# Performance work log

Measured on AMD Instinct MI355X. Metric: run time of the kernel, lower is better.

Reference implementation:

```python
import jax, jax.numpy as jnp
import numpy as np

C = 128
EPS = 1e-5


def _ln(x, g, b):
    m = jnp.mean(x, axis=-1, keepdims=True)
    v = jnp.mean((x - m) ** 2, axis=-1, keepdims=True)
    return (x - m) * jax.lax.rsqrt(v + EPS) * g + b


def setup_inputs() -> dict:
    key = jax.random.key(0)
    ks = jax.random.split(key, 10)
    B, N = 1, 384
    s = 1.0 / np.sqrt(C)
    inp = {
        "z": jax.random.normal(ks[0], (B, N, N, C), dtype=jnp.float32),
        "ln1_g": jnp.ones((C,), jnp.float32),
        "ln1_b": jnp.zeros((C,), jnp.float32),
        "ln2_g": jnp.ones((C,), jnp.float32),
        "ln2_b": jnp.zeros((C,), jnp.float32),
        "Wa": jax.random.uniform(ks[1], (C, C), jnp.float32, -s, s),
        "ba": jnp.zeros((C,), jnp.float32),
        "Wga": jax.random.uniform(ks[2], (C, C), jnp.float32, -s, s),
        "bga": jnp.zeros((C,), jnp.float32),
        "Wb": jax.random.uniform(ks[3], (C, C), jnp.float32, -s, s),
        "bb": jnp.zeros((C,), jnp.float32),
        "Wgb": jax.random.uniform(ks[4], (C, C), jnp.float32, -s, s),
        "bgb": jnp.zeros((C,), jnp.float32),
        "Wg": jax.random.uniform(ks[5], (C, C), jnp.float32, -s, s),
        "bg": jnp.zeros((C,), jnp.float32),
        "Wo": jax.random.uniform(ks[6], (C, C), jnp.float32, -s, s),
        "bo": jnp.zeros((C,), jnp.float32),
    }
    return inp


def reference(z, ln1_g, ln1_b, ln2_g, ln2_b, Wa, ba, Wga, bga, Wb, bb, Wgb, bgb, Wg, bg, Wo, bo):
    # z: (B, i, j, c)
    zn = _ln(z, ln1_g, ln1_b)
    a = (zn @ Wa + ba) * jax.nn.sigmoid(zn @ Wga + bga)      # (B,i,k,c)
    b = (zn @ Wb + bb) * jax.nn.sigmoid(zn @ Wgb + bgb)      # (B,j,k,c)
    gate = jax.nn.sigmoid(zn @ Wg + bg)                      # (B,i,j,c)
    o = jnp.einsum('bikc,bjkc->bijc', a, b)                  # outgoing triangle update
    return gate * (_ln(o, ln2_g, ln2_b) @ Wo + bo)
```

## Files before the change

kernel.cpp:

```cpp
#include <hip/hip_runtime.h>
#include <stdint.h>

typedef _Float16 f16x8 __attribute__((ext_vector_type(8)));
typedef float floatx4 __attribute__((ext_vector_type(4)));

#define RR 147456
#define NC 128
#define NN 384

__device__ inline floatx4 zero4() { floatx4 v; v[0]=0.f; v[1]=0.f; v[2]=0.f; v[3]=0.f; return v; }
__device__ inline float sigmoidf_(float x) { return 1.f / (1.f + __expf(-x)); }

__global__ __launch_bounds__(256) void k0_wt(
    const float* __restrict__ w0, const float* __restrict__ w1,
    const float* __restrict__ w2, const float* __restrict__ w3,
    const float* __restrict__ w4, const float* __restrict__ w5,
    _Float16* __restrict__ wf)
{
  const float* w;
  switch (blockIdx.x) {
    case 0: w = w0; break; case 1: w = w1; break; case 2: w = w2; break;
    case 3: w = w3; break; case 4: w = w4; break; default: w = w5; break;
  }
  _Float16* out = wf + blockIdx.x * 16384;
  const int t = threadIdx.x;
  for (int it = 0; it < 64; ++it) {
    int f = it * 256 + t;
    int j  = f & 7;
    int ln = (f >> 3) & 63;
    int nt = (f >> 9) & 7;
    int k0 = f >> 12;
    int k = k0 * 32 + (ln >> 4) * 8 + j;
    int n = nt * 16 + (ln & 15);
    out[f] = (_Float16)w[k * 128 + n];
  }
}

__global__ __launch_bounds__(256, 4) void k2_ln_gemm(
    const float* __restrict__ z, const float* __restrict__ ln1g, const float* __restrict__ ln1b,
    const _Float16* __restrict__ wf,
    const float* __restrict__ ba, const float* __restrict__ bga,
    const float* __restrict__ bb, const float* __restrict__ bgb,
    const float* __restrict__ bg,
    _Float16* __restrict__ at, _Float16* __restrict__ bt, _Float16* __restrict__ gate)
{
  __shared__ __align__(16) _Float16 zns[64][136];
  __shared__ __align__(16) _Float16 bnc[4][32 * 72];
  const int t = threadIdx.x;
  const int w = t >> 6, lane = t & 63;
  const int l15 = lane & 15, quad = lane >> 4;
  const int r0 = blockIdx.x * 64;
  const int nt0 = w * 2;

  {
    const int g = lane >> 4, h = lane & 15;
    float4 ga = *(const float4*)(ln1g + h*8);
    float4 gb = *(const float4*)(ln1g + h*8 + 4);
    float4 bba = *(const float4*)(ln1b + h*8);
    float4 bbb = *(const float4*)(ln1b + h*8 + 4);
    #pragma unroll
    for (int rr = 0; rr < 4; ++rr) {
      int row = w * 16 + rr * 4 + g;
      const float* zp = z + (size_t)(r0 + row) * NC + h * 8;
      float4 xa = *(const float4*)zp;
      float4 xb = *(const float4*)(zp + 4);
      float s = xa.x + xa.y + xa.z + xa.w + xb.x + xb.y + xb.z + xb.w;
      float q = xa.x*xa.x + xa.y*xa.y + xa.z*xa.z + xa.w*xa.w
              + xb.x*xb.x + xb.y*xb.y + xb.z*xb.z + xb.w*xb.w;
      #pragma unroll
      for (int m = 1; m < 16; m <<= 1) { s += __shfl_xor(s, m); q += __shfl_xor(q, m); }
      float mean = s * (1.f/128.f);
      float var  = q * (1.f/128.f) - mean*mean;
      float rs = rsqrtf(var + 1e-5f);
      union { uint4 u; _Float16 hh[8]; } pk;
      pk.hh[0] = (_Float16)((xa.x - mean) * rs * ga.x + bba.x);
      pk.hh[1] = (_Float16)((xa.y - mean) * rs * ga.y + bba.y);
      pk.hh[2] = (_Float16)((xa.z - mean) * rs * ga.z + bba.z);
      pk.hh[3] = (_Float16)((xa.w - mean) * rs * ga.w + bba.w);
      pk.hh[4] = (_Float16)((xb.x - mean) * rs * gb.x + bbb.x);
      pk.hh[5] = (_Float16)((xb.y - mean) * rs * gb.y + bbb.y);
      pk.hh[6] = (_Float16)((xb.z - mean) * rs * gb.z + bbb.z);
      pk.hh[7] = (_Float16)((xb.w - mean) * rs * gb.w + bbb.w);
      *(uint4*)&zns[row][h * 8] = pk.u;
    }
  }
  __syncthreads();

  const _Float16* pw = wf + lane * 8;
  f16x8 bw[4][2];
  floatx4 acc[4][2];
  union PkU { unsigned int u; _Float16 h[2]; };
  PkU sig[4][2][2];

  auto loadw = [&](int slot) {
    const _Float16* p = pw + slot * 16384;
    #pragma unroll
    for (int k0 = 0; k0 < 4; ++k0)
      #pragma unroll
      for (int j = 0; j < 2; ++j)
        bw[k0][j] = *(const f16x8*)(p + (k0*8 + nt0 + j) * 512);
  };
  auto dogemm = [&]() {
    #pragma unroll
    for (int mt = 0; mt < 4; ++mt) {
      acc[mt][0] = zero4(); acc[mt][1] = zero4();
      #pragma unroll
      for (int k0 = 0; k0 < 4; ++k0) {
        f16x8 af = *(const f16x8*)&zns[mt*16 + l15][k0*32 + quad*8];
        acc[mt][0] = __builtin_amdgcn_mfma_f32_16x16x32_f16(af, bw[k0][0], acc[mt][0], 0, 0, 0);
        acc[mt][1] = __builtin_amdgcn_mfma_f32_16x16x32_f16(af, bw[k0][1], acc[mt][1], 0, 0, 0);
      }
    }
  };
  auto sigpack = [&](const float* big) {
    #pragma unroll
    for (int j = 0; j < 2; ++j) {
      float bgv = big[(nt0 + j)*16 + l15];
      #pragma unroll
      for (int mt = 0; mt < 4; ++mt) {
        sig[mt][j][0].h[0] = (_Float16)sigmoidf_(acc[mt][j][0] + bgv);
        sig[mt][j][0].h[1] = (_Float16)sigmoidf_(acc[mt][j][1] + bgv);
        sig[mt][j][1].h[0] = (_Float16)sigmoidf_(acc[mt][j][2] + bgv);
        sig[mt][j][1].h[1] = (_Float16)sigmoidf_(acc[mt][j][3] + bgv);
      }
    }
  };
  auto bounce_out = [&](_Float16* dst) {
    asm volatile("s_waitcnt lgkmcnt(0)" ::: "memory");
    const int q2 = lane & 3, cl = lane >> 2;
    #pragma unroll
    for (int i = 0; i < 4; ++i) {
      int cp  = cl + (i >> 1) * 16;
      int ofs = (i & 1) * 32 + q2 * 8;
      uint4 v = *(const uint4*)&bnc[w][cp * 72 + ofs];
      *(uint4*)(dst + (size_t)(w*32 + cp) * RR + r0 + ofs) = v;
    }
  };
  auto combine_store = [&](const float* bia, _Float16* dst) {
    #pragma unroll
    for (int j = 0; j < 2; ++j) {
      int c = (nt0 + j)*16 + l15;
      float bav = bia[c];
      #pragma unroll
      for (int mt = 0; mt < 4; ++mt) {
        union { uint2 u2; _Float16 h[4]; } pk;
        pk.h[0] = (_Float16)((acc[mt][j][0] + bav) * (float)sig[mt][j][0].h[0]);
        pk.h[1] = (_Float16)((acc[mt][j][1] + bav) * (float)sig[mt][j][0].h[1]);
        pk.h[2] = (_Float16)((acc[mt][j][2] + bav) * (float)sig[mt][j][1].h[0]);
        pk.h[3] = (_Float16)((acc[mt][j][3] + bav) * (float)sig[mt][j][1].h[1]);
        *(uint2*)&bnc[w][(j*16 + l15) * 72 + mt*16 + quad*4] = pk.u2;
      }
    }
    bounce_out(dst);
  };

  loadw(1); dogemm(); sigpack(bga);
  loadw(0); dogemm();
  loadw(3);
  combine_store(ba, at);
  dogemm(); sigpack(bgb);
  loadw(2); dogemm();
  loadw(4);
  combine_store(bb, bt);
  dogemm();
  #pragma unroll
  for (int j = 0; j < 2; ++j) {
    float bgv = bg[(nt0 + j)*16 + l15];
    #pragma unroll
    for (int mt = 0; mt < 4; ++mt) {
      union { uint2 u2; _Float16 h[4]; } pk;
      #pragma unroll
      for (int r = 0; r < 4; ++r)
        pk.h[r] = (_Float16)sigmoidf_(acc[mt][j][r] + bgv);
      *(uint2*)&bnc[w][(j*16 + l15) * 72 + mt*16 + quad*4] = pk.u2;
    }
  }
  bounce_out(gate);
}

__global__ __launch_bounds__(256, 3) void k3_tri(
    const _Float16* __restrict__ at, const _Float16* __restrict__ bt, _Float16* __restrict__ o)
{
  __shared__ __align__(16) _Float16 As[2][128 * 40];
  __shared__ __align__(16) _Float16 Bs[2][128 * 40];
  const int t = threadIdx.x;
  const int w = t >> 6, lane = t & 63, l15 = lane & 15, quad = lane >> 4;
  const int c = blockIdx.y;
  const int i0 = (blockIdx.x / 3) * 128, j0 = (blockIdx.x % 3) * 128;
  const int wi = w >> 1, wj = w & 1;
  const size_t base = (size_t)c * RR;
  const _Float16* A  = at + base;
  const _Float16* Bp = bt + base;

  const int srow = t >> 1, sch = (t & 1) * 16;
  const _Float16* ga = A  + (size_t)(i0 + srow) * NN + sch;
  const _Float16* gb = Bp + (size_t)(j0 + srow) * NN + sch;
  _Float16* const pa0 = &As[0][srow * 40 + sch];
  _Float16* const pb0 = &Bs[0][srow * 40 + sch];
  _Float16* const pa1 = &As[1][srow * 40 + sch];
  _Float16* const pb1 = &Bs[1][srow * 40 + sch];

  floatx4 acc[4][4];
  #pragma unroll
  for (int mt = 0; mt < 4; ++mt)
    #pragma unroll
    for (int nt = 0; nt < 4; ++nt) acc[mt][nt] = zero4();

  f16x8 aP0,aP1,bP0,bP1, aQ0,aQ1,bQ0,bQ1;

  auto gloadP = [&](int kk) {
    aP0 = *(const f16x8*)(ga + kk); aP1 = *(const f16x8*)(ga + kk + 8);
    bP0 = *(const f16x8*)(gb + kk); bP1 = *(const f16x8*)(gb + kk + 8);
  };
  auto gloadQ = [&](int kk) {
    aQ0 = *(const f16x8*)(ga + kk); aQ1 = *(const f16x8*)(ga + kk + 8);
    bQ0 = *(const f16x8*)(gb + kk); bQ1 = *(const f16x8*)(gb + kk + 8);
  };
  auto swriteP = [&](int buf) {
    _Float16* pa = buf ? pa1 : pa0; _Float16* pb = buf ? pb1 : pb0;
    *(f16x8*)pa = aP0; *(f16x8*)(pa + 8) = aP1;
    *(f16x8*)pb = bP0; *(f16x8*)(pb + 8) = bP1;
  };
  auto swriteQ = [&](int buf) {
    _Float16* pa = buf ? pa1 : pa0; _Float16* pb = buf ? pb1 : pb0;
    *(f16x8*)pa = aQ0; *(f16x8*)(pa + 8) = aQ1;
    *(f16x8*)pb = bQ0; *(f16x8*)(pb + 8) = bQ1;
  };
  auto compute = [&](int buf) {
    f16x8 af[4], bfr[4];
    #pragma unroll
    for (int mt = 0; mt < 4; ++mt)
      af[mt] = *(const f16x8*)&As[buf][(wi*64 + mt*16 + l15) * 40 + quad*8];
    #pragma unroll
    for (int nt = 0; nt < 4; ++nt)
      bfr[nt] = *(const f16x8*)&Bs[buf][(wj*64 + nt*16 + l15) * 40 + quad*8];
    #pragma unroll
    for (int mt = 0; mt < 4; ++mt)
      #pragma unroll
      for (int nt = 0; nt < 4; ++nt)
        acc[mt][nt] = __builtin_amdgcn_mfma_f32_16x16x32_f16(af[mt], bfr[nt], acc[mt][nt], 0, 0, 0);
  };

  gloadP(0); swriteP(0); gloadP(32);
  __syncthreads();
  #pragma unroll
  for (int s = 0; s < 12; s += 2) {
    if (s + 2 < 12) gloadQ((s + 2) * 32);
    compute(0);
    swriteP(1);
    __syncthreads();
    if (s + 3 < 12) gloadP((s + 3) * 32);
    compute(1);
    if (s + 2 < 12) { swriteQ(0); __syncthreads(); }
  }

  #pragma unroll
  for (int mt = 0; mt < 4; ++mt) {
    #pragma unroll
    for (int r = 0; r < 4; ++r) {
      int i = i0 + wi*64 + mt*16 + quad*4 + r;
      _Float16* orow = o + base + (size_t)i * NN + j0 + wj*64;
      #pragma unroll
      for (int nt = 0; nt < 4; ++nt) orow[nt*16 + l15] = (_Float16)acc[mt][nt][r];
    }
  }
}

__global__ __launch_bounds__(256, 4) void k4_out(
    const _Float16* __restrict__ o, const _Float16* __restrict__ gate,
    const float* __restrict__ ln2g, const float* __restrict__ ln2b,
    const _Float16* __restrict__ wo5, const float* __restrict__ bo,
    float* __restrict__ out)
{
  __shared__ __align__(16) _Float16 osb[64][136];
  const int t = threadIdx.x;
  const int w = t >> 6, lane = t & 63, l15 = lane & 15, quad = lane >> 4;
  const int r0 = blockIdx.x * 64;
  const int nt0 = w * 2;

  #pragma unroll
  for (int it = 0; it < 4; ++it) {
    int f = (it * 256 + t) * 8;
    int cx = f >> 6, p = f & 63;
    f16x8 v = *(const f16x8*)(o + (size_t)cx * RR + r0 + p);
    #pragma unroll
    for (int i = 0; i < 8; ++i) osb[p + i][cx] = v[i];
  }
  __syncthreads();

  {
    const int g = lane >> 4, h = lane & 15;
    float4 ga = *(const float4*)(ln2g + h*8);
    float4 gb = *(const float4*)(ln2g + h*8 + 4);
    float4 bba = *(const float4*)(ln2b + h*8);
    float4 bbb = *(const float4*)(ln2b + h*8 + 4);
    #pragma unroll
    for (int rr = 0; rr < 4; ++rr) {
      int row = w * 16 + rr * 4 + g;
      f16x8 xv = *(const f16x8*)&osb[row][h*8];
      float x0 = (float)xv[0], x1 = (float)xv[1], x2 = (float)xv[2], x3 = (float)xv[3];
      float x4 = (float)xv[4], x5 = (float)xv[5], x6 = (float)xv[6], x7 = (float)xv[7];
      float s = x0+x1+x2+x3+x4+x5+x6+x7;
      float q = x0*x0+x1*x1+x2*x2+x3*x3+x4*x4+x5*x5+x6*x6+x7*x7;
      #pragma unroll
      for (int m = 1; m < 16; m <<= 1) { s += __shfl_xor(s, m); q += __shfl_xor(q, m); }
      float mean = s * (1.f/128.f);
      float var  = q * (1.f/128.f) - mean*mean;
      float rs = rsqrtf(var + 1e-5f);
      union { uint4 u; _Float16 hh[8]; } pk;
      pk.hh[0] = (_Float16)((x0 - mean) * rs * ga.x + bba.x);
      pk.hh[1] = (_Float16)((x1 - mean) * rs * ga.y + bba.y);
      pk.hh[2] = (_Float16)((x2 - mean) * rs * ga.z + bba.z);
      pk.hh[3] = (_Float16)((x3 - mean) * rs * ga.w + bba.w);
      pk.hh[4] = (_Float16)((x4 - mean) * rs * gb.x + bbb.x);
      pk.hh[5] = (_Float16)((x5 - mean) * rs * gb.y + bbb.y);
      pk.hh[6] = (_Float16)((x6 - mean) * rs * gb.z + bbb.z);
      pk.hh[7] = (_Float16)((x7 - mean) * rs * gb.w + bbb.w);
      *(uint4*)&osb[row][h * 8] = pk.u;
    }
  }
  __syncthreads();

  f16x8 bw[4][2];
  {
    const _Float16* p = wo5 + lane * 8;
    #pragma unroll
    for (int k0 = 0; k0 < 4; ++k0)
      #pragma unroll
      for (int j = 0; j < 2; ++j)
        bw[k0][j] = *(const f16x8*)(p + (k0*8 + nt0 + j) * 512);
  }
  floatx4 acc[4][2];
  #pragma unroll
  for (int mt = 0; mt < 4; ++mt) {
    acc[mt][0] = zero4(); acc[mt][1] = zero4();
    #pragma unroll
    for (int k0 = 0; k0 < 4; ++k0) {
      f16x8 af = *(const f16x8*)&osb[mt*16 + l15][k0*32 + quad*8];
      acc[mt][0] = __builtin_amdgcn_mfma_f32_16x16x32_f16(af, bw[k0][0], acc[mt][0], 0, 0, 0);
      acc[mt][1] = __builtin_amdgcn_mfma_f32_16x16x32_f16(af, bw[k0][1], acc[mt][1], 0, 0, 0);
    }
  }

  #pragma unroll
  for (int j = 0; j < 2; ++j) {
    int cch = (nt0 + j)*16 + l15;
    float bov = bo[cch];
    #pragma unroll
    for (int mt = 0; mt < 4; ++mt) {
      union { uint2 u2; _Float16 h[4]; } gk;
      gk.u2 = *(const uint2*)(gate + (size_t)cch * RR + r0 + mt*16 + quad*4);
      #pragma unroll
      for (int r = 0; r < 4; ++r) {
        int rl = mt*16 + quad*4 + r;
        out[(size_t)(r0 + rl) * NC + cch] = (float)gk.h[r] * (acc[mt][j][r] + bov);
      }
    }
  }
}

extern "C" void kernel_launch(void* const* d_in, const int* in_sizes, int n_in,
                              void* d_out, int out_size, void* d_ws, size_t ws_size,
                              hipStream_t stream) {
  const float* z    = (const float*)d_in[0];
  const float* l1g  = (const float*)d_in[1];
  const float* l1b  = (const float*)d_in[2];
  const float* l2g  = (const float*)d_in[3];
  const float* l2b  = (const float*)d_in[4];
  const float* Wa   = (const float*)d_in[5];
  const float* ba   = (const float*)d_in[6];
  const float* Wga  = (const float*)d_in[7];
  const float* bga  = (const float*)d_in[8];
  const float* Wb   = (const float*)d_in[9];
  const float* bb   = (const float*)d_in[10];
  const float* Wgb  = (const float*)d_in[11];
  const float* bgb  = (const float*)d_in[12];
  const float* Wg   = (const float*)d_in[13];
  const float* bg   = (const float*)d_in[14];
  const float* Wo   = (const float*)d_in[15];
  const float* bo   = (const float*)d_in[16];

  char* ws = (char*)d_ws;
  _Float16* at_  = (_Float16*)(ws + 0);
  _Float16* bt_  = (_Float16*)(ws + 37748736);
  _Float16* gate = (_Float16*)(ws + 75497472);
  _Float16* o16  = (_Float16*)(ws + 113246208);
  _Float16* wf   = (_Float16*)(ws + 188743680);

  hipLaunchKernelGGL(k0_wt, dim3(6), dim3(256), 0, stream, Wa, Wga, Wb, Wgb, Wg, Wo, wf);
  hipLaunchKernelGGL(k2_ln_gemm, dim3(2304), dim3(256), 0, stream,
                     z, l1g, l1b, wf, ba, bga, bb, bgb, bg, at_, bt_, gate);
  hipLaunchKernelGGL(k3_tri, dim3(9, 128), dim3(256), 0, stream, at_, bt_, o16);
  hipLaunchKernelGGL(k4_out, dim3(2304), dim3(256), 0, stream,
                     o16, gate, l2g, l2b, wf + 5*16384, bo, (float*)d_out);
}
```

Measured before the change: 329.1 us.

## Switch intermediates to blocked 64-position-by-channel tile layout

Intermediate tensors (a, b, gate, o) move from a channel-major layout with stride RR to a blocked layout. Each 64-position block stores all 128 channels contiguously as 8192-element tiles. Stores from the projection kernel and loads in the output kernel become fully contiguous 16KB chunks instead of 128 strided rows. The triangle kernel's K-loop loads now cross tile boundaries every 64 elements, and its output stores are reindexed to match.

```diff
diff --git a/kernel.cpp b/kernel.cpp
--- a/kernel.cpp
+++ b/kernel.cpp
@@ -127,13 +127,13 @@
   };
   auto bounce_out = [&](_Float16* dst) {
     asm volatile("s_waitcnt lgkmcnt(0)" ::: "memory");
-    const int q2 = lane & 3, cl = lane >> 2;
+    _Float16* base = dst + (size_t)blockIdx.x * 8192 + w * 2048;
     #pragma unroll
     for (int i = 0; i < 4; ++i) {
-      int cp  = cl + (i >> 1) * 16;
-      int ofs = (i & 1) * 32 + q2 * 8;
-      uint4 v = *(const uint4*)&bnc[w][cp * 72 + ofs];
-      *(uint4*)(dst + (size_t)(w*32 + cp) * RR + r0 + ofs) = v;
+      int f = i * 512 + lane * 8;
+      int cp = f >> 6, pos = f & 63;
+      uint4 v = *(const uint4*)&bnc[w][cp * 72 + pos];
+      *(uint4*)(base + f) = v;
     }
   };
   auto combine_store = [&](const float* bia, _Float16* dst) {
@@ -188,13 +188,10 @@
   const int c = blockIdx.y;
   const int i0 = (blockIdx.x / 3) * 128, j0 = (blockIdx.x % 3) * 128;
   const int wi = w >> 1, wj = w & 1;
-  const size_t base = (size_t)c * RR;
-  const _Float16* A  = at + base;
-  const _Float16* Bp = bt + base;
 
   const int srow = t >> 1, sch = (t & 1) * 16;
-  const _Float16* ga = A  + (size_t)(i0 + srow) * NN + sch;
-  const _Float16* gb = Bp + (size_t)(j0 + srow) * NN + sch;
+  const _Float16* gaRow = at + (size_t)(i0 + srow) * 6 * 8192 + (size_t)c * 64;
+  const _Float16* gbRow = bt + (size_t)(j0 + srow) * 6 * 8192 + (size_t)c * 64;
   _Float16* const pa0 = &As[0][srow * 40 + sch];
   _Float16* const pb0 = &Bs[0][srow * 40 + sch];
   _Float16* const pa1 = &As[1][srow * 40 + sch];
@@ -208,13 +205,19 @@
 
   f16x8 aP0,aP1,bP0,bP1, aQ0,aQ1,bQ0,bQ1;
 
+  auto gofs = [&](int kk) -> size_t {
+    int x = kk + sch;
+    return (size_t)(x >> 6) * 8192 + (size_t)(x & 63);
+  };
   auto gloadP = [&](int kk) {
-    aP0 = *(const f16x8*)(ga + kk); aP1 = *(const f16x8*)(ga + kk + 8);
-    bP0 = *(const f16x8*)(gb + kk); bP1 = *(const f16x8*)(gb + kk + 8);
+    size_t go = gofs(kk);
+    aP0 = *(const f16x8*)(gaRow + go); aP1 = *(const f16x8*)(gaRow + go + 8);
+    bP0 = *(const f16x8*)(gbRow + go); bP1 = *(const f16x8*)(gbRow + go + 8);
   };
   auto gloadQ = [&](int kk) {
-    aQ0 = *(const f16x8*)(ga + kk); aQ1 = *(const f16x8*)(ga + kk + 8);
-    bQ0 = *(const f16x8*)(gb + kk); bQ1 = *(const f16x8*)(gb + kk + 8);
+    size_t go = gofs(kk);
+    aQ0 = *(const f16x8*)(gaRow + go); aQ1 = *(const f16x8*)(gaRow + go + 8);
+    bQ0 = *(const f16x8*)(gbRow + go); bQ1 = *(const f16x8*)(gbRow + go + 8);
   };
   auto swriteP = [&](int buf) {
     _Float16* pa = buf ? pa1 : pa0; _Float16* pb = buf ? pb1 : pb0;
@@ -259,9 +262,9 @@
     #pragma unroll
     for (int r = 0; r < 4; ++r) {
       int i = i0 + wi*64 + mt*16 + quad*4 + r;
-      _Float16* orow = o + base + (size_t)i * NN + j0 + wj*64;
-      #pragma unroll
-      for (int nt = 0; nt < 4; ++nt) orow[nt*16 + l15] = (_Float16)acc[mt][nt][r];
+      _Float16* obase = o + (size_t)(i*6 + (j0 >> 6) + wj) * 8192 + (size_t)c * 64;
+      #pragma unroll
+      for (int nt = 0; nt < 4; ++nt) obase[nt*16 + l15] = (_Float16)acc[mt][nt][r];
     }
   }
 }
@@ -278,13 +281,16 @@
   const int r0 = blockIdx.x * 64;
   const int nt0 = w * 2;
 
-  #pragma unroll
-  for (int it = 0; it < 4; ++it) {
-    int f = (it * 256 + t) * 8;
-    int cx = f >> 6, p = f & 63;
-    f16x8 v = *(const f16x8*)(o + (size_t)cx * RR + r0 + p);
-    #pragma unroll
-    for (int i = 0; i < 8; ++i) osb[p + i][cx] = v[i];
+  {
+    const _Float16* ob = o + (size_t)blockIdx.x * 8192;
+    #pragma unroll
+    for (int it = 0; it < 4; ++it) {
+      int f = (it * 256 + t) * 8;
+      int cx = f >> 6, p = f & 63;
+      f16x8 v = *(const f16x8*)(ob + f);
+      #pragma unroll
+      for (int i = 0; i < 8; ++i) osb[p + i][cx] = v[i];
+    }
   }
   __syncthreads();
 
@@ -349,7 +355,7 @@
     #pragma unroll
     for (int mt = 0; mt < 4; ++mt) {
       union { uint2 u2; _Float16 h[4]; } gk;
-      gk.u2 = *(const uint2*)(gate + (size_t)cch * RR + r0 + mt*16 + quad*4);
+      gk.u2 = *(const uint2*)(gate + (size_t)blockIdx.x * 8192 + (size_t)cch * 64 + mt*16 + quad*4);
       #pragma unroll
       for (int r = 0; r < 4; ++r) {
         int rl = mt*16 + quad*4 + r;
```

Result: no change. 323.2 us (-1.8%).
